# Kernel optimization log

Hardware: AMD Instinct MI355X
Metric: run time of the kernel (lower is better)

## Reference

```python
import jax, jax.numpy as jnp
import numpy as np

B, N_ELEC, N_NUC, D_EMB, D_MSG = 512, 32, 8, 128, 128


def idx_perm(n):
    # ordered pairs (i, j), i != j, shaped [n, n-1]
    i = np.repeat(np.arange(n), n - 1).reshape(n, n - 1)
    j = np.array([[k for k in range(n) if k != ii] for ii in range(n)])
    return jnp.asarray(i), jnp.asarray(j)


def pairwise_diffs(a, b):
    # a: [..., n, 3], b: [..., m, 3] -> [..., n, m, 4] (dx, dy, dz, |d|^2)
    d = a[..., :, None, :] - b[..., None, :, :]
    return jnp.concatenate([d, jnp.sum(d * d, axis=-1, keepdims=True)], axis=-1)


def mlp(x, w1, b1, w2, b2):
    return jax.nn.silu(x @ w1 + b1) @ w2 + b2


def setup_inputs() -> dict:
    key = jax.random.key(0)
    ks = jax.random.split(key, 10)
    sc = 0.1
    return {
        'rs': jax.random.normal(ks[0], (B, N_ELEC, 3), jnp.float32),
        'coords': jax.random.normal(ks[1], (N_NUC, 3), jnp.float32),
        'messages_el': jax.random.normal(ks[2], (B, N_ELEC, N_ELEC - 1, D_MSG), jnp.float32),
        'messages_nuc': jax.random.normal(ks[3], (B, N_ELEC, N_NUC, D_MSG), jnp.float32),
        'emb': jax.random.normal(ks[4], (B, N_ELEC, D_EMB), jnp.float32),
        'w1_el': jax.random.normal(ks[5], (D_EMB + D_MSG, 256), jnp.float32) * sc,
        'b1_el': jnp.zeros((256,), jnp.float32),
        'w2_el': jax.random.normal(ks[6], (256, 1), jnp.float32) * sc,
        'b2_el': jnp.zeros((1,), jnp.float32),
        'w1_nuc': jax.random.normal(ks[7], (D_EMB + D_MSG, 256), jnp.float32) * sc,
        'b1_nuc': jnp.zeros((256,), jnp.float32),
        'w2_nuc': jax.random.normal(ks[8], (256, 1), jnp.float32) * sc,
        'b2_nuc': jnp.zeros((1,), jnp.float32),
        'nuc_charges': jnp.array([6.0, 1.0, 1.0, 1.0, 1.0, 1.0, 1.0, 1.0], jnp.float32),
    }


def reference(rs, coords, messages_el, messages_nuc, emb,
              w1_el, b1_el, w2_el, b2_el,
              w1_nuc, b1_nuc, w2_nuc, b2_nuc, nuc_charges):
    n_elec, n_nuc = rs.shape[-2], coords.shape[0]
    emb_p = emb[:, :, None]  # [B, n_elec, 1, D_emb]
    # gather-concat features per pair
    f_el = jnp.concatenate(
        [jnp.broadcast_to(emb_p, (B, n_elec, n_elec - 1, D_EMB)), messages_el], axis=-1)
    f_nuc = jnp.concatenate(
        [jnp.broadcast_to(emb_p, (B, n_elec, n_nuc, D_EMB)), messages_nuc], axis=-1)
    i, j = idx_perm(n_elec)
    diffs_nuc = pairwise_diffs(rs, coords)  # [B, n_elec, n_nuc, 4]
    diffs_ee = pairwise_diffs(-rs, -rs)[:, i, j]  # [B, n_elec, n_elec-1, 4]
    diffs = jnp.concatenate([diffs_ee, diffs_nuc], axis=-2)
    f = jnp.concatenate(
        [mlp(f_el, w1_el, b1_el, w2_el, b2_el),
         mlp(f_nuc, w1_nuc, b1_nuc, w2_nuc, b2_nuc)], axis=-2)  # [B, n_elec, P, 1]
    ps = f * diffs[..., :3] / (1.0 + diffs[..., 3:] ** 1.5)
    ps = ps.sum(axis=-2)  # [B, n_elec, 3]
    # deeperwin decay
    decay = jnp.tanh(diffs_nuc[..., -1] / (0.5 / nuc_charges) ** 2).prod(axis=-1)
    return np.exp(-3.5).astype(np.float32) * decay[..., None] * ps
```

## Files before the change

kernel.cpp:

```cpp
#include <hip/hip_runtime.h>
#include <hip/hip_bf16.h>

#define OUT_SCALE 0.030197383422318501f

typedef __attribute__((ext_vector_type(8))) short bf16x8;
typedef __attribute__((ext_vector_type(4))) float f32x4;

#define EL_BLOCKS 2048
#define NUC_BLOCKS 2048

__device__ __forceinline__ unsigned pk2(float a, float b) {
  __hip_bfloat162 h = __float22bfloat162_rn(make_float2(a, b));
  unsigned u;
  __builtin_memcpy(&u, &h, 4);
  return u;
}

__device__ __forceinline__ float silu_f(float h) {
  return h * __builtin_amdgcn_rcpf(1.0f + __expf(-h));
}

__global__ void prep_w1(const float* __restrict__ w1a,
                        const float* __restrict__ w1b,
                        unsigned short* __restrict__ wp) {
  int gid = blockIdx.x * 256 + threadIdx.x;
  const float* w1 = (gid < 8192) ? w1a : w1b;
  int rem = gid & 8191;
  int kk = rem >> 10;
  int kg = (rem >> 8) & 3;
  int col = rem & 255;
  const float* src = w1 + (kk * 32 + kg * 8) * 256 + col;
  uint4 v;
  v.x = pk2(src[0 * 256], src[1 * 256]);
  v.y = pk2(src[2 * 256], src[3 * 256]);
  v.z = pk2(src[4 * 256], src[5 * 256]);
  v.w = pk2(src[6 * 256], src[7 * 256]);
  *(uint4*)(wp + (size_t)gid * 8) = v;
}

__global__ __launch_bounds__(512, 4) void bf_main_kernel(
    const float* __restrict__ rs, const float* __restrict__ msg_el,
    const float* __restrict__ msg_nuc, const float* __restrict__ emb,
    const unsigned short* __restrict__ wpk,
    const float* __restrict__ b1_el, const float* __restrict__ w2_el,
    const float* __restrict__ b2_el,
    const float* __restrict__ b1_nuc, const float* __restrict__ w2_nuc,
    const float* __restrict__ b2_nuc,
    const float* __restrict__ coords, const float* __restrict__ chg,
    float* __restrict__ out) {
  __shared__ __align__(16) unsigned short s_emb[16 * 128];
  __shared__ __align__(16) unsigned short s_msg[2 * 32 * 128];
  __shared__ __align__(16) float s_embc[8 * 256];
  __shared__ __align__(16) float s_w2[256];
  __shared__ float s_fp[8][256];
  __shared__ float s_ps[8][4];
  __shared__ float s_decay[8];

  const int tid = threadIdx.x;
  const int bid = blockIdx.x;
  const int lane = tid & 63;
  const int wv = tid >> 6;
  const int cIdx = lane & 15, kg = lane >> 4;
  const int lr = tid >> 4, ch2 = tid & 15;

  if (bid < EL_BLOCKS) {
    const int gp0 = bid * 8;
    const float* msg = msg_el;

    if (tid < 32) ((float*)s_ps)[tid] = 0.0f;

    {
      int p = tid >> 4, ch = tid & 15;
      if (tid < 128) {
        const float* src = emb + (gp0 + p) * 128 + ch * 8;
        float4 v0 = *(const float4*)src;
        float4 v1 = *(const float4*)(src + 4);
        uint4 pk;
        pk.x = pk2(v0.x, v0.y); pk.y = pk2(v0.z, v0.w);
        pk.z = pk2(v1.x, v1.y); pk.w = pk2(v1.z, v1.w);
        *(uint4*)(s_emb + p * 128 + (ch ^ p) * 8) = pk;
      } else if (tid < 256) {
        uint4 z = {0u, 0u, 0u, 0u};
        *(uint4*)(s_emb + p * 128 + (ch ^ (p & 15)) * 8) = z;
      }
      if (tid < 256) s_w2[tid] = w2_el[tid];
    }

    bf16x8 Bf[4][2];
    const int col = wv * 32 + cIdx;
#pragma unroll
    for (int nt = 0; nt < 2; ++nt)
#pragma unroll
      for (int kk = 0; kk < 4; ++kk)
        Bf[kk][nt] = *(const bf16x8*)(
            wpk + (size_t)((kk * 4 + kg) * 256 + col + nt * 16) * 8);

    const int jc = (lr < 31) ? lr : 30;
    const float* mptr = msg + (size_t)(gp0 * 31 + jc) * 128 + ch2 * 8;
    float4 la = *(const float4*)mptr;
    float4 lb = *(const float4*)(mptr + 4);
    mptr += 31 * 128;

    __syncthreads();

    {
      f32x4 aE0 = {0, 0, 0, 0}, aE1 = {0, 0, 0, 0};
#pragma unroll
      for (int kk = 0; kk < 4; ++kk) {
        bf16x8 a = *(const bf16x8*)(
            s_emb + cIdx * 128 + ((kk * 4 + kg) ^ cIdx) * 8);
        aE0 = __builtin_amdgcn_mfma_f32_16x16x32_bf16(Bf[kk][0], a, aE0, 0, 0, 0);
        aE1 = __builtin_amdgcn_mfma_f32_16x16x32_bf16(Bf[kk][1], a, aE1, 0, 0, 0);
      }
      if (cIdx < 8) {
        f32x4 b1a = *(const f32x4*)(b1_el + wv * 32 + kg * 4);
        f32x4 b1b = *(const f32x4*)(b1_el + wv * 32 + 16 + kg * 4);
        *(f32x4*)(s_embc + cIdx * 256 + wv * 32 + kg * 4) = aE0 + b1a;
        *(f32x4*)(s_embc + cIdx * 256 + wv * 32 + 16 + kg * 4) = aE1 + b1b;
      }
    }

#pragma unroll
    for (int nt = 0; nt < 2; ++nt)
#pragma unroll
      for (int kk = 0; kk < 4; ++kk)
        Bf[kk][nt] = *(const bf16x8*)(
            wpk + (size_t)(((kk + 4) * 4 + kg) * 256 + col + nt * 16) * 8);

    {
      uint4 pk;
      pk.x = pk2(la.x, la.y); pk.y = pk2(la.z, la.w);
      pk.z = pk2(lb.x, lb.y); pk.w = pk2(lb.z, lb.w);
      *(uint4*)(s_msg + lr * 128 + ((ch2 ^ (lr & 15)) * 8)) = pk;
    }

    __syncthreads();

#pragma unroll 1
    for (int c = 0; c < 8; ++c) {
      if (c < 7) {
        la = *(const float4*)mptr;
        lb = *(const float4*)(mptr + 4);
        mptr += 31 * 128;
      }
      const unsigned short* mb = s_msg + (c & 1) * 4096;
      const float* ec = s_embc + c * 256;
#pragma unroll
      for (int tt = 0; tt < 2; ++tt) {
        f32x4 acc0 = *(const f32x4*)(ec + wv * 32 + kg * 4);
        f32x4 acc1 = *(const f32x4*)(ec + wv * 32 + 16 + kg * 4);
        const unsigned short* mp = mb + (tt * 16 + cIdx) * 128;
#pragma unroll
        for (int kk = 0; kk < 4; ++kk) {
          bf16x8 a = *(const bf16x8*)(mp + ((kk * 4 + kg) ^ cIdx) * 8);
          acc0 = __builtin_amdgcn_mfma_f32_16x16x32_bf16(Bf[kk][0], a, acc0, 0, 0, 0);
          acc1 = __builtin_amdgcn_mfma_f32_16x16x32_bf16(Bf[kk][1], a, acc1, 0, 0, 0);
        }
        f32x4 w2a = *(const f32x4*)(s_w2 + wv * 32 + kg * 4);
        f32x4 w2b = *(const f32x4*)(s_w2 + wv * 32 + 16 + kg * 4);
        float p0 = 0.0f, p1 = 0.0f;
#pragma unroll
        for (int reg = 0; reg < 4; ++reg) {
          p0 += silu_f(acc0[reg]) * w2a[reg];
          p1 += silu_f(acc1[reg]) * w2b[reg];
        }
        float v = p0 + p1;
        v += __shfl_xor(v, 16);
        v += __shfl_xor(v, 32);
        if (kg == 0) s_fp[wv][(c * 2 + tt) * 16 + cIdx] = v;
      }
      if (c < 7) {
        uint4 pk;
        pk.x = pk2(la.x, la.y); pk.y = pk2(la.z, la.w);
        pk.z = pk2(lb.x, lb.y); pk.w = pk2(lb.z, lb.w);
        *(uint4*)(s_msg + ((c + 1) & 1) * 4096 + lr * 128 +
                  ((ch2 ^ (lr & 15)) * 8)) = pk;
      }
      __syncthreads();
    }

    if (tid < 248) {
      int p = tid / 31, jj = tid - p * 31;
      int gp = gp0 + p, b = gp >> 5, i = gp & 31;
      int jidx = jj + (jj >= i ? 1 : 0);
      const float* rsb = rs + b * 96;
      float dx = rsb[jidx * 3 + 0] - rsb[i * 3 + 0];
      float dy = rsb[jidx * 3 + 1] - rsb[i * 3 + 1];
      float dz = rsb[jidx * 3 + 2] - rsb[i * 3 + 2];
      float tq = dx * dx + dy * dy + dz * dz;
      int row = p * 32 + jj;
      float f = b2_el[0];
#pragma unroll
      for (int w = 0; w < 8; ++w) f += s_fp[w][row];
      float g = f * __builtin_amdgcn_rcpf(1.0f + tq * sqrtf(tq));
      atomicAdd(&s_ps[p][0], g * dx);
      atomicAdd(&s_ps[p][1], g * dy);
      atomicAdd(&s_ps[p][2], g * dz);
    }
    if (tid < 8) {
      int gp = gp0 + tid, b = gp >> 5, i = gp & 31;
      float x = rs[(b * 32 + i) * 3 + 0];
      float y = rs[(b * 32 + i) * 3 + 1];
      float z = rs[(b * 32 + i) * 3 + 2];
      float dcy = 1.0f;
#pragma unroll
      for (int n = 0; n < 8; ++n) {
        float dx = x - coords[n * 3 + 0];
        float dy = y - coords[n * 3 + 1];
        float dz = z - coords[n * 3 + 2];
        float tq = dx * dx + dy * dy + dz * dz;
        float zc = chg[n];
        dcy *= tanhf(4.0f * tq * zc * zc);
      }
      s_decay[tid] = dcy;
    }
    __syncthreads();
    if (tid < 24) {
      int p = tid / 3, c = tid - p * 3;
      int gp = gp0 + p;
      atomicAdd(&out[gp * 3 + c], OUT_SCALE * s_decay[p] * s_ps[p][c]);
    }
  } else {
    const int nbid = bid - EL_BLOCKS;
    const int gp0 = nbid * 8;
    const float* msg = msg_nuc;
    const unsigned short* wp = wpk + 8192 * 8;

    if (tid < 32) ((float*)s_ps)[tid] = 0.0f;

    {
      int p = tid >> 4, ch = tid & 15;
      if (tid < 128) {
        const float* src = emb + (gp0 + p) * 128 + ch * 8;
        float4 v0 = *(const float4*)src;
        float4 v1 = *(const float4*)(src + 4);
        uint4 pk;
        pk.x = pk2(v0.x, v0.y); pk.y = pk2(v0.z, v0.w);
        pk.z = pk2(v1.x, v1.y); pk.w = pk2(v1.z, v1.w);
        *(uint4*)(s_emb + p * 128 + (ch ^ p) * 8) = pk;
      } else if (tid < 256) {
        uint4 z = {0u, 0u, 0u, 0u};
        *(uint4*)(s_emb + p * 128 + (ch ^ (p & 15)) * 8) = z;
      }
      if (tid < 256) s_w2[tid] = w2_nuc[tid];
    }

    bf16x8 Bf[4][2];
    const int col = wv * 32 + cIdx;
#pragma unroll
    for (int nt = 0; nt < 2; ++nt)
#pragma unroll
      for (int kk = 0; kk < 4; ++kk)
        Bf[kk][nt] = *(const bf16x8*)(
            wp + (size_t)((kk * 4 + kg) * 256 + col + nt * 16) * 8);

    const float* mptr = msg + (size_t)(gp0 * 8 + lr) * 128 + ch2 * 8;
    float4 la = *(const float4*)mptr;
    float4 lb = *(const float4*)(mptr + 4);
    mptr += 32 * 128;

    __syncthreads();

    {
      f32x4 aE0 = {0, 0, 0, 0}, aE1 = {0, 0, 0, 0};
#pragma unroll
      for (int kk = 0; kk < 4; ++kk) {
        bf16x8 a = *(const bf16x8*)(
            s_emb + cIdx * 128 + ((kk * 4 + kg) ^ cIdx) * 8);
        aE0 = __builtin_amdgcn_mfma_f32_16x16x32_bf16(Bf[kk][0], a, aE0, 0, 0, 0);
        aE1 = __builtin_amdgcn_mfma_f32_16x16x32_bf16(Bf[kk][1], a, aE1, 0, 0, 0);
      }
      if (cIdx < 8) {
        f32x4 b1a = *(const f32x4*)(b1_nuc + wv * 32 + kg * 4);
        f32x4 b1b = *(const f32x4*)(b1_nuc + wv * 32 + 16 + kg * 4);
        *(f32x4*)(s_embc + cIdx * 256 + wv * 32 + kg * 4) = aE0 + b1a;
        *(f32x4*)(s_embc + cIdx * 256 + wv * 32 + 16 + kg * 4) = aE1 + b1b;
      }
    }

#pragma unroll
    for (int nt = 0; nt < 2; ++nt)
#pragma unroll
      for (int kk = 0; kk < 4; ++kk)
        Bf[kk][nt] = *(const bf16x8*)(
            wp + (size_t)(((kk + 4) * 4 + kg) * 256 + col + nt * 16) * 8);

    {
      uint4 pk;
      pk.x = pk2(la.x, la.y); pk.y = pk2(la.z, la.w);
      pk.z = pk2(lb.x, lb.y); pk.w = pk2(lb.z, lb.w);
      *(uint4*)(s_msg + lr * 128 + ((ch2 ^ (lr & 15)) * 8)) = pk;
    }

    __syncthreads();

#pragma unroll 1
    for (int c = 0; c < 2; ++c) {
      if (c < 1) {
        la = *(const float4*)mptr;
        lb = *(const float4*)(mptr + 4);
      }
      const unsigned short* mb = s_msg + (c & 1) * 4096;
#pragma unroll
      for (int tt = 0; tt < 2; ++tt) {
        int p = 4 * c + 2 * tt + (cIdx >> 3);
        const float* ec = s_embc + p * 256;
        f32x4 acc0 = *(const f32x4*)(ec + wv * 32 + kg * 4);
        f32x4 acc1 = *(const f32x4*)(ec + wv * 32 + 16 + kg * 4);
        const unsigned short* mp = mb + (tt * 16 + cIdx) * 128;
#pragma unroll
        for (int kk = 0; kk < 4; ++kk) {
          bf16x8 a = *(const bf16x8*)(mp + ((kk * 4 + kg) ^ cIdx) * 8);
          acc0 = __builtin_amdgcn_mfma_f32_16x16x32_bf16(Bf[kk][0], a, acc0, 0, 0, 0);
          acc1 = __builtin_amdgcn_mfma_f32_16x16x32_bf16(Bf[kk][1], a, acc1, 0, 0, 0);
        }
        f32x4 w2a = *(const f32x4*)(s_w2 + wv * 32 + kg * 4);
        f32x4 w2b = *(const f32x4*)(s_w2 + wv * 32 + 16 + kg * 4);
        float p0 = 0.0f, p1 = 0.0f;
#pragma unroll
        for (int reg = 0; reg < 4; ++reg) {
          p0 += silu_f(acc0[reg]) * w2a[reg];
          p1 += silu_f(acc1[reg]) * w2b[reg];
        }
        float v = p0 + p1;
        v += __shfl_xor(v, 16);
        v += __shfl_xor(v, 32);
        if (kg == 0) s_fp[wv][(c * 2 + tt) * 16 + cIdx] = v;
      }
      if (c < 1) {
        uint4 pk;
        pk.x = pk2(la.x, la.y); pk.y = pk2(la.z, la.w);
        pk.z = pk2(lb.x, lb.y); pk.w = pk2(lb.z, lb.w);
        *(uint4*)(s_msg + 4096 + lr * 128 + ((ch2 ^ (lr & 15)) * 8)) = pk;
      }
      __syncthreads();
    }

    if (tid < 64) {
      int p = tid >> 3, n = tid & 7;
      int gp = gp0 + p, b = gp >> 5, i = gp & 31;
      float dx = rs[(b * 32 + i) * 3 + 0] - coords[n * 3 + 0];
      float dy = rs[(b * 32 + i) * 3 + 1] - coords[n * 3 + 1];
      float dz = rs[(b * 32 + i) * 3 + 2] - coords[n * 3 + 2];
      float tq = dx * dx + dy * dy + dz * dz;
      float f = b2_nuc[0];
#pragma unroll
      for (int w = 0; w < 8; ++w) f += s_fp[w][tid];
      float g = f * __builtin_amdgcn_rcpf(1.0f + tq * sqrtf(tq));
      atomicAdd(&s_ps[p][0], g * dx);
      atomicAdd(&s_ps[p][1], g * dy);
      atomicAdd(&s_ps[p][2], g * dz);
    }
    if (tid < 8) {
      int gp = gp0 + tid, b = gp >> 5, i = gp & 31;
      float x = rs[(b * 32 + i) * 3 + 0];
      float y = rs[(b * 32 + i) * 3 + 1];
      float z = rs[(b * 32 + i) * 3 + 2];
      float dcy = 1.0f;
#pragma unroll
      for (int n = 0; n < 8; ++n) {
        float dx = x - coords[n * 3 + 0];
        float dy = y - coords[n * 3 + 1];
        float dz = z - coords[n * 3 + 2];
        float tq = dx * dx + dy * dy + dz * dz;
        float zc = chg[n];
        dcy *= tanhf(4.0f * tq * zc * zc);
      }
      s_decay[tid] = dcy;
    }
    __syncthreads();
    if (tid < 24) {
      int p = tid / 3, c = tid - p * 3;
      int gp = gp0 + p;
      atomicAdd(&out[gp * 3 + c], OUT_SCALE * s_decay[p] * s_ps[p][c]);
    }
  }
}

extern "C" void kernel_launch(void* const* d_in, const int* in_sizes, int n_in,
                              void* d_out, int out_size, void* d_ws, size_t ws_size,
                              hipStream_t stream) {
  const float* rs       = (const float*)d_in[0];
  const float* coords   = (const float*)d_in[1];
  const float* msg_el   = (const float*)d_in[2];
  const float* msg_nuc  = (const float*)d_in[3];
  const float* emb      = (const float*)d_in[4];
  const float* w1_el    = (const float*)d_in[5];
  const float* b1_el    = (const float*)d_in[6];
  const float* w2_el    = (const float*)d_in[7];
  const float* b2_el    = (const float*)d_in[8];
  const float* w1_nuc   = (const float*)d_in[9];
  const float* b1_nuc   = (const float*)d_in[10];
  const float* w2_nuc   = (const float*)d_in[11];
  const float* b2_nuc   = (const float*)d_in[12];
  const float* chg      = (const float*)d_in[13];
  float* out = (float*)d_out;

  unsigned short* wpk = (unsigned short*)d_ws;

  hipMemsetAsync(out, 0, (size_t)out_size * sizeof(float), stream);
  prep_w1<<<64, 256, 0, stream>>>(w1_el, w1_nuc, wpk);
  bf_main_kernel<<<EL_BLOCKS + NUC_BLOCKS, 512, 0, stream>>>(
      rs, msg_el, msg_nuc, emb, wpk, b1_el, w2_el, b2_el, b1_nuc, w2_nuc,
      b2_nuc, coords, chg, out);
}
```

Baseline: 132.0 us.

## Give each wave its own electron pair set and loop over hidden columns

Work is now split across waves by electron (one wave per electron) rather than by hidden column. Each wave loads and converts all of its electron's message rows into a private LDS slice, then walks all 16 hidden column tiles, streaming the W1 fragments from global memory per tile. This removes the per-chunk block barriers, the double-buffered message pipeline and the 8-way cross-wave s_fp reduction. In exchange, LDS grows to 64 KB for messages, which may lower occupancy, and W1 fragments are reloaded for every column tile instead of being held in registers.

```diff
diff --git a/kernel.cpp b/kernel.cpp
--- a/kernel.cpp
+++ b/kernel.cpp
@@ -49,10 +49,10 @@
     const float* __restrict__ coords, const float* __restrict__ chg,
     float* __restrict__ out) {
   __shared__ __align__(16) unsigned short s_emb[16 * 128];
-  __shared__ __align__(16) unsigned short s_msg[2 * 32 * 128];
+  __shared__ __align__(16) unsigned short s_msg[8 * 32 * 128];
   __shared__ __align__(16) float s_embc[8 * 256];
   __shared__ __align__(16) float s_w2[256];
-  __shared__ float s_fp[8][256];
+  __shared__ float s_fp[256];
   __shared__ float s_ps[8][4];
   __shared__ float s_decay[8];
 
@@ -61,7 +61,6 @@
   const int lane = tid & 63;
   const int wv = tid >> 6;
   const int cIdx = lane & 15, kg = lane >> 4;
-  const int lr = tid >> 4, ch2 = tid & 15;
 
   if (bid < EL_BLOCKS) {
     const int gp0 = bid * 8;
@@ -86,24 +85,17 @@
       if (tid < 256) s_w2[tid] = w2_el[tid];
     }
 
-    bf16x8 Bf[4][2];
-    const int col = wv * 32 + cIdx;
-#pragma unroll
-    for (int nt = 0; nt < 2; ++nt)
-#pragma unroll
-      for (int kk = 0; kk < 4; ++kk)
-        Bf[kk][nt] = *(const bf16x8*)(
-            wpk + (size_t)((kk * 4 + kg) * 256 + col + nt * 16) * 8);
-
-    const int jc = (lr < 31) ? lr : 30;
-    const float* mptr = msg + (size_t)(gp0 * 31 + jc) * 128 + ch2 * 8;
-    float4 la = *(const float4*)mptr;
-    float4 lb = *(const float4*)(mptr + 4);
-    mptr += 31 * 128;
-
     __syncthreads();
 
     {
+      const int col = wv * 32 + cIdx;
+      bf16x8 Bf[4][2];
+#pragma unroll
+      for (int nt = 0; nt < 2; ++nt)
+#pragma unroll
+        for (int kk = 0; kk < 4; ++kk)
+          Bf[kk][nt] = *(const bf16x8*)(
+              wpk + (size_t)((kk * 4 + kg) * 256 + col + nt * 16) * 8);
       f32x4 aE0 = {0, 0, 0, 0}, aE1 = {0, 0, 0, 0};
 #pragma unroll
       for (int kk = 0; kk < 4; ++kk) {
@@ -120,85 +112,81 @@
       }
     }
 
-#pragma unroll
-    for (int nt = 0; nt < 2; ++nt)
+    __syncthreads();
+
+    const int gp = gp0 + wv;
+    unsigned short* myms = s_msg + wv * 4096;
+
+#pragma unroll 4
+    for (int u = 0; u < 8; ++u) {
+      int id = u * 64 + lane;
+      int row = id >> 4, ch = id & 15;
+      int jc = row < 31 ? row : 30;
+      const float* s = msg + (size_t)(gp * 31 + jc) * 128 + ch * 8;
+      float4 a = *(const float4*)s;
+      float4 b = *(const float4*)(s + 4);
+      uint4 pk;
+      pk.x = pk2(a.x, a.y); pk.y = pk2(a.z, a.w);
+      pk.z = pk2(b.x, b.y); pk.w = pk2(b.z, b.w);
+      *(uint4*)(myms + row * 128 + ((ch ^ (row & 15)) * 8)) = pk;
+    }
+
+    const unsigned short* mp0 = myms + cIdx * 128;
+    const unsigned short* mp1 = myms + (16 + cIdx) * 128;
+    const float* ec = s_embc + wv * 256;
+    float part0 = 0.0f, part1 = 0.0f;
+#pragma unroll 2
+    for (int ph = 0; ph < 16; ++ph) {
+      bf16x8 Bq[4];
 #pragma unroll
       for (int kk = 0; kk < 4; ++kk)
-        Bf[kk][nt] = *(const bf16x8*)(
-            wpk + (size_t)(((kk + 4) * 4 + kg) * 256 + col + nt * 16) * 8);
-
-    {
-      uint4 pk;
-      pk.x = pk2(la.x, la.y); pk.y = pk2(la.z, la.w);
-      pk.z = pk2(lb.x, lb.y); pk.w = pk2(lb.z, lb.w);
-      *(uint4*)(s_msg + lr * 128 + ((ch2 ^ (lr & 15)) * 8)) = pk;
-    }
-
-    __syncthreads();
-
-#pragma unroll 1
-    for (int c = 0; c < 8; ++c) {
-      if (c < 7) {
-        la = *(const float4*)mptr;
-        lb = *(const float4*)(mptr + 4);
-        mptr += 31 * 128;
-      }
-      const unsigned short* mb = s_msg + (c & 1) * 4096;
-      const float* ec = s_embc + c * 256;
-#pragma unroll
-      for (int tt = 0; tt < 2; ++tt) {
-        f32x4 acc0 = *(const f32x4*)(ec + wv * 32 + kg * 4);
-        f32x4 acc1 = *(const f32x4*)(ec + wv * 32 + 16 + kg * 4);
-        const unsigned short* mp = mb + (tt * 16 + cIdx) * 128;
-#pragma unroll
-        for (int kk = 0; kk < 4; ++kk) {
-          bf16x8 a = *(const bf16x8*)(mp + ((kk * 4 + kg) ^ cIdx) * 8);
-          acc0 = __builtin_amdgcn_mfma_f32_16x16x32_bf16(Bf[kk][0], a, acc0, 0, 0, 0);
-          acc1 = __builtin_amdgcn_mfma_f32_16x16x32_bf16(Bf[kk][1], a, acc1, 0, 0, 0);
-        }
-        f32x4 w2a = *(const f32x4*)(s_w2 + wv * 32 + kg * 4);
-        f32x4 w2b = *(const f32x4*)(s_w2 + wv * 32 + 16 + kg * 4);
-        float p0 = 0.0f, p1 = 0.0f;
-#pragma unroll
-        for (int reg = 0; reg < 4; ++reg) {
-          p0 += silu_f(acc0[reg]) * w2a[reg];
-          p1 += silu_f(acc1[reg]) * w2b[reg];
-        }
-        float v = p0 + p1;
-        v += __shfl_xor(v, 16);
-        v += __shfl_xor(v, 32);
-        if (kg == 0) s_fp[wv][(c * 2 + tt) * 16 + cIdx] = v;
-      }
-      if (c < 7) {
-        uint4 pk;
-        pk.x = pk2(la.x, la.y); pk.y = pk2(la.z, la.w);
-        pk.z = pk2(lb.x, lb.y); pk.w = pk2(lb.z, lb.w);
-        *(uint4*)(s_msg + ((c + 1) & 1) * 4096 + lr * 128 +
-                  ((ch2 ^ (lr & 15)) * 8)) = pk;
-      }
-      __syncthreads();
-    }
+        Bq[kk] = *(const bf16x8*)(
+            wpk + (size_t)(((kk + 4) * 4 + kg) * 256 + ph * 16 + cIdx) * 8);
+      f32x4 init = *(const f32x4*)(ec + ph * 16 + kg * 4);
+      f32x4 acc0 = init, acc1 = init;
+#pragma unroll
+      for (int kk = 0; kk < 4; ++kk) {
+        int sw = ((kk * 4 + kg) ^ cIdx) * 8;
+        bf16x8 a0 = *(const bf16x8*)(mp0 + sw);
+        bf16x8 a1 = *(const bf16x8*)(mp1 + sw);
+        acc0 = __builtin_amdgcn_mfma_f32_16x16x32_bf16(Bq[kk], a0, acc0, 0, 0, 0);
+        acc1 = __builtin_amdgcn_mfma_f32_16x16x32_bf16(Bq[kk], a1, acc1, 0, 0, 0);
+      }
+      f32x4 w2v = *(const f32x4*)(s_w2 + ph * 16 + kg * 4);
+#pragma unroll
+      for (int r = 0; r < 4; ++r) {
+        part0 += silu_f(acc0[r]) * w2v[r];
+        part1 += silu_f(acc1[r]) * w2v[r];
+      }
+    }
+    part0 += __shfl_xor(part0, 16);
+    part0 += __shfl_xor(part0, 32);
+    part1 += __shfl_xor(part1, 16);
+    part1 += __shfl_xor(part1, 32);
+    if (kg == 0) {
+      s_fp[wv * 32 + cIdx] = part0;
+      s_fp[wv * 32 + 16 + cIdx] = part1;
+    }
+
+    __syncthreads();
 
     if (tid < 248) {
       int p = tid / 31, jj = tid - p * 31;
-      int gp = gp0 + p, b = gp >> 5, i = gp & 31;
+      int gpx = gp0 + p, b = gpx >> 5, i = gpx & 31;
       int jidx = jj + (jj >= i ? 1 : 0);
       const float* rsb = rs + b * 96;
       float dx = rsb[jidx * 3 + 0] - rsb[i * 3 + 0];
       float dy = rsb[jidx * 3 + 1] - rsb[i * 3 + 1];
       float dz = rsb[jidx * 3 + 2] - rsb[i * 3 + 2];
       float tq = dx * dx + dy * dy + dz * dz;
-      int row = p * 32 + jj;
-      float f = b2_el[0];
-#pragma unroll
-      for (int w = 0; w < 8; ++w) f += s_fp[w][row];
+      float f = s_fp[p * 32 + jj] + b2_el[0];
       float g = f * __builtin_amdgcn_rcpf(1.0f + tq * sqrtf(tq));
       atomicAdd(&s_ps[p][0], g * dx);
       atomicAdd(&s_ps[p][1], g * dy);
       atomicAdd(&s_ps[p][2], g * dz);
     }
     if (tid < 8) {
-      int gp = gp0 + tid, b = gp >> 5, i = gp & 31;
+      int gpx = gp0 + tid, b = gpx >> 5, i = gpx & 31;
       float x = rs[(b * 32 + i) * 3 + 0];
       float y = rs[(b * 32 + i) * 3 + 1];
       float z = rs[(b * 32 + i) * 3 + 2];
@@ -217,8 +205,8 @@
     __syncthreads();
     if (tid < 24) {
       int p = tid / 3, c = tid - p * 3;
-      int gp = gp0 + p;
-      atomicAdd(&out[gp * 3 + c], OUT_SCALE * s_decay[p] * s_ps[p][c]);
+      int gpx = gp0 + p;
+      atomicAdd(&out[gpx * 3 + c], OUT_SCALE * s_decay[p] * s_ps[p][c]);
     }
   } else {
     const int nbid = bid - EL_BLOCKS;
@@ -245,23 +233,17 @@
       if (tid < 256) s_w2[tid] = w2_nuc[tid];
     }
 
-    bf16x8 Bf[4][2];
-    const int col = wv * 32 + cIdx;
-#pragma unroll
-    for (int nt = 0; nt < 2; ++nt)
-#pragma unroll
-      for (int kk = 0; kk < 4; ++kk)
-        Bf[kk][nt] = *(const bf16x8*)(
-            wp + (size_t)((kk * 4 + kg) * 256 + col + nt * 16) * 8);
-
-    const float* mptr = msg + (size_t)(gp0 * 8 + lr) * 128 + ch2 * 8;
-    float4 la = *(const float4*)mptr;
-    float4 lb = *(const float4*)(mptr + 4);
-    mptr += 32 * 128;
-
     __syncthreads();
 
     {
+      const int col = wv * 32 + cIdx;
+      bf16x8 Bf[4][2];
+#pragma unroll
+      for (int nt = 0; nt < 2; ++nt)
+#pragma unroll
+        for (int kk = 0; kk < 4; ++kk)
+          Bf[kk][nt] = *(const bf16x8*)(
+              wp + (size_t)((kk * 4 + kg) * 256 + col + nt * 16) * 8);
       f32x4 aE0 = {0, 0, 0, 0}, aE1 = {0, 0, 0, 0};
 #pragma unroll
       for (int kk = 0; kk < 4; ++kk) {
@@ -278,81 +260,70 @@
       }
     }
 
-#pragma unroll
-    for (int nt = 0; nt < 2; ++nt)
+    __syncthreads();
+
+    unsigned short* myms = s_msg + wv * 4096;
+#pragma unroll
+    for (int u = 0; u < 2; ++u) {
+      int id = u * 64 + lane;
+      int row = 8 + (id >> 4), ch = id & 15;
+      uint4 z = {0u, 0u, 0u, 0u};
+      *(uint4*)(myms + row * 128 + ch * 8) = z;
+    }
+#pragma unroll
+    for (int u = 0; u < 2; ++u) {
+      int id = u * 64 + lane;
+      int row = id >> 4, ch = id & 15;
+      const float* s = msg + (size_t)((gp0 + wv) * 8 + row) * 128 + ch * 8;
+      float4 a = *(const float4*)s;
+      float4 b = *(const float4*)(s + 4);
+      uint4 pk;
+      pk.x = pk2(a.x, a.y); pk.y = pk2(a.z, a.w);
+      pk.z = pk2(b.x, b.y); pk.w = pk2(b.z, b.w);
+      *(uint4*)(myms + row * 128 + ((ch ^ row) * 8)) = pk;
+    }
+
+    const unsigned short* mp0 = myms + cIdx * 128;
+    const float* ec = s_embc + wv * 256;
+    float part0 = 0.0f;
+#pragma unroll 2
+    for (int ph = 0; ph < 16; ++ph) {
+      bf16x8 Bq[4];
 #pragma unroll
       for (int kk = 0; kk < 4; ++kk)
-        Bf[kk][nt] = *(const bf16x8*)(
-            wp + (size_t)(((kk + 4) * 4 + kg) * 256 + col + nt * 16) * 8);
-
-    {
-      uint4 pk;
-      pk.x = pk2(la.x, la.y); pk.y = pk2(la.z, la.w);
-      pk.z = pk2(lb.x, lb.y); pk.w = pk2(lb.z, lb.w);
-      *(uint4*)(s_msg + lr * 128 + ((ch2 ^ (lr & 15)) * 8)) = pk;
-    }
-
-    __syncthreads();
-
-#pragma unroll 1
-    for (int c = 0; c < 2; ++c) {
-      if (c < 1) {
-        la = *(const float4*)mptr;
-        lb = *(const float4*)(mptr + 4);
-      }
-      const unsigned short* mb = s_msg + (c & 1) * 4096;
-#pragma unroll
-      for (int tt = 0; tt < 2; ++tt) {
-        int p = 4 * c + 2 * tt + (cIdx >> 3);
-        const float* ec = s_embc + p * 256;
-        f32x4 acc0 = *(const f32x4*)(ec + wv * 32 + kg * 4);
-        f32x4 acc1 = *(const f32x4*)(ec + wv * 32 + 16 + kg * 4);
-        const unsigned short* mp = mb + (tt * 16 + cIdx) * 128;
-#pragma unroll
-        for (int kk = 0; kk < 4; ++kk) {
-          bf16x8 a = *(const bf16x8*)(mp + ((kk * 4 + kg) ^ cIdx) * 8);
-          acc0 = __builtin_amdgcn_mfma_f32_16x16x32_bf16(Bf[kk][0], a, acc0, 0, 0, 0);
-          acc1 = __builtin_amdgcn_mfma_f32_16x16x32_bf16(Bf[kk][1], a, acc1, 0, 0, 0);
-        }
-        f32x4 w2a = *(const f32x4*)(s_w2 + wv * 32 + kg * 4);
-        f32x4 w2b = *(const f32x4*)(s_w2 + wv * 32 + 16 + kg * 4);
-        float p0 = 0.0f, p1 = 0.0f;
-#pragma unroll
-        for (int reg = 0; reg < 4; ++reg) {
-          p0 += silu_f(acc0[reg]) * w2a[reg];
-          p1 += silu_f(acc1[reg]) * w2b[reg];
-        }
-        float v = p0 + p1;
-        v += __shfl_xor(v, 16);
-        v += __shfl_xor(v, 32);
-        if (kg == 0) s_fp[wv][(c * 2 + tt) * 16 + cIdx] = v;
-      }
-      if (c < 1) {
-        uint4 pk;
-        pk.x = pk2(la.x, la.y); pk.y = pk2(la.z, la.w);
-        pk.z = pk2(lb.x, lb.y); pk.w = pk2(lb.z, lb.w);
-        *(uint4*)(s_msg + 4096 + lr * 128 + ((ch2 ^ (lr & 15)) * 8)) = pk;
-      }
-      __syncthreads();
-    }
+        Bq[kk] = *(const bf16x8*)(
+            wp + (size_t)(((kk + 4) * 4 + kg) * 256 + ph * 16 + cIdx) * 8);
+      f32x4 acc0 = *(const f32x4*)(ec + ph * 16 + kg * 4);
+#pragma unroll
+      for (int kk = 0; kk < 4; ++kk) {
+        bf16x8 a0 = *(const bf16x8*)(mp0 + ((kk * 4 + kg) ^ cIdx) * 8);
+        acc0 = __builtin_amdgcn_mfma_f32_16x16x32_bf16(Bq[kk], a0, acc0, 0, 0, 0);
+      }
+      f32x4 w2v = *(const f32x4*)(s_w2 + ph * 16 + kg * 4);
+#pragma unroll
+      for (int r = 0; r < 4; ++r) part0 += silu_f(acc0[r]) * w2v[r];
+    }
+    part0 += __shfl_xor(part0, 16);
+    part0 += __shfl_xor(part0, 32);
+    if (kg == 0 && cIdx < 8) s_fp[wv * 8 + cIdx] = part0;
+
+    __syncthreads();
 
     if (tid < 64) {
       int p = tid >> 3, n = tid & 7;
-      int gp = gp0 + p, b = gp >> 5, i = gp & 31;
+      int gpx = gp0 + p, b = gpx >> 5, i = gpx & 31;
       float dx = rs[(b * 32 + i) * 3 + 0] - coords[n * 3 + 0];
       float dy = rs[(b * 32 + i) * 3 + 1] - coords[n * 3 + 1];
       float dz = rs[(b * 32 + i) * 3 + 2] - coords[n * 3 + 2];
       float tq = dx * dx + dy * dy + dz * dz;
-      float f = b2_nuc[0];
-#pragma unroll
-      for (int w = 0; w < 8; ++w) f += s_fp[w][tid];
+      float f = s_fp[tid] + b2_nuc[0];
       float g = f * __builtin_amdgcn_rcpf(1.0f + tq * sqrtf(tq));
       atomicAdd(&s_ps[p][0], g * dx);
       atomicAdd(&s_ps[p][1], g * dy);
       atomicAdd(&s_ps[p][2], g * dz);
     }
     if (tid < 8) {
-      int gp = gp0 + tid, b = gp >> 5, i = gp & 31;
+      int gpx = gp0 + tid, b = gpx >> 5, i = gpx & 31;
       float x = rs[(b * 32 + i) * 3 + 0];
       float y = rs[(b * 32 + i) * 3 + 1];
       float z = rs[(b * 32 + i) * 3 + 2];
@@ -371,8 +342,8 @@
     __syncthreads();
     if (tid < 24) {
       int p = tid / 3, c = tid - p * 3;
-      int gp = gp0 + p;
-      atomicAdd(&out[gp * 3 + c], OUT_SCALE * s_decay[p] * s_ps[p][c]);
+      int gpx = gp0 + p;
+      atomicAdd(&out[gpx * 3 + c], OUT_SCALE * s_decay[p] * s_ps[p][c]);
     }
   }
 }
```

Result: slower. 157.6 us (+19.4%).
